# Kernel tuning notes

Hardware: AMD Instinct MI355X
Metric: run time of the kernel (lower is better)

The kernel has to match this reference:

```python
import jax, jax.numpy as jnp
import numpy as np

IN_CH = 128
OUT_CH = 256
KSIZE = 3
DOWN = 2
WSCALE_GAIN = 1.0
LR_MUL = 1.0
ACT_GAIN = float(np.sqrt(2.0))  # lrelu def_gain
CONV_CLAMP = 256.0
LRELU_SLOPE = 0.2


def _setup_filter():
    # upfirdn2d.setup_filter([1,3,3,1]): normalize 1D then outer product -> 2D
    f1 = jnp.asarray([1.0, 3.0, 3.0, 1.0], dtype=jnp.float32)
    f1 = f1 / jnp.sum(f1)
    f2 = jnp.outer(f1, f1)  # [4,4]
    return f2


def setup_inputs() -> dict:
    key = jax.random.key(0)
    k1, k2 = jax.random.split(key)
    x = jax.random.normal(k1, (16, IN_CH, 256, 256), dtype=jnp.float32)
    weight = jax.random.normal(k2, (OUT_CH, IN_CH, KSIZE, KSIZE), dtype=jnp.float32)
    bias = jnp.zeros((OUT_CH,), dtype=jnp.float32)
    return {"x": x, "weight": weight, "bias": bias}


def reference(x, weight, bias):
    # runtime_gain = 1.0
    fan_in = KSIZE * KSIZE * IN_CH
    wscale = WSCALE_GAIN / np.sqrt(fan_in) * LR_MUL  # use_wscale=True
    w = weight * jnp.float32(wscale)
    b = bias * jnp.float32(LR_MUL)

    # filter_padding for k=3, fh=fw=4, down=2 -> (2,2,2,2) as (left,right,top,bottom)
    pad = (KSIZE // 2 + (4 - DOWN + 1) // 2, KSIZE // 2 + (4 - DOWN) // 2)
    # upfirdn2d(x, f, down=1, padding): pad then correlate with flipped filter
    f2 = _setup_filter()
    f2 = f2[::-1, ::-1]  # flip (symmetric here, kept for faithfulness)
    C = x.shape[1]
    fk = jnp.broadcast_to(f2[None, None], (C, 1, 4, 4))  # depthwise kernel
    x = lax.pad_fn(x, pad) if False else jnp.pad(x, ((0, 0), (0, 0), (pad[1], pad[0]) if False else (pad[0], pad[1]), (pad[0], pad[1])))
    x = jax.lax.conv_general_dilated(
        x, fk, window_strides=(1, 1), padding='VALID',
        dimension_numbers=('NCHW', 'OIHW', 'NCHW'),
        feature_group_count=C)

    # strided conv2d, padding=0, stride=down
    x = jax.lax.conv_general_dilated(
        x, w, window_strides=(DOWN, DOWN), padding='VALID',
        dimension_numbers=('NCHW', 'OIHW', 'NCHW'))

    # fused bias + lrelu + gain + clamp
    x = x + b[None, :, None, None]
    x = jnp.where(x >= 0, x, x * jnp.float32(LRELU_SLOPE)) * jnp.float32(ACT_GAIN)
    x = jnp.clip(x, -jnp.float32(CONV_CLAMP), jnp.float32(CONV_CLAMP))
    return x
```

## Files before the change

### kernel.cpp

```cpp
#include <hip/hip_runtime.h>

typedef __attribute__((ext_vector_type(8))) short bf16x8;
typedef __attribute__((ext_vector_type(4))) float f32x4;
typedef __attribute__((ext_vector_type(2))) float f32x2;
typedef __attribute__((ext_vector_type(4))) unsigned int u32x4;

static __device__ __forceinline__ unsigned short f2bf(float f) {
    union { float f; unsigned u; } v; v.f = f;
    return (unsigned short)((v.u + 0x7FFFu + ((v.u >> 16) & 1u)) >> 16);
}

__global__ void prep_weights(const float* __restrict__ w, unsigned short* __restrict__ wp) {
    int t = blockIdx.x * 256 + threadIdx.x;
    const float wscale = 0.02946278254943948f;
    int cw = t & 31;
    int oc = (t >> 5) & 255;
    int cr = t >> 13;
    int ch = cr / 9;
    int rs = cr - ch * 9;
    int r  = rs / 3;
    int s  = rs - r * 3;
    int c  = ch * 32 + cw;
    wp[t] = f2bf(w[((oc * 128 + c) * 3 + r) * 3 + s] * wscale);
}

__global__ __launch_bounds__(256, 2)
void blur_pre(const float* __restrict__ x, unsigned* __restrict__ bm, unsigned* __restrict__ bs) {
    const int b = blockIdx.x;
    const int tband = b & 15;
    const int chpg  = (b >> 4) & 3;
    const int cg    = (b >> 6) & 3;
    const int n     = b >> 8;
    const int wv = threadIdx.x >> 6;
    const int L  = threadIdx.x & 63;
    const int chp = chpg * 4 + wv;
    const float* p0 = x + (size_t)(n * 128 + cg * 32 + 2 * chp) * 65536;
    const float* p1 = p0 + 65536;
    const int t0 = tband * 16;
    const int J0 = 4 * L;
    const bool L0 = (L == 0), L63 = (L == 63);
    const int colA = L0 ? 0 : (J0 - 2);
    const int colB = L63 ? 252 : (J0 + 2);
    unsigned* ob = bm + (size_t)((n * 4 + cg) * 16 + chp) * 65792;
    unsigned* os = bs + (size_t)((n * 4 + cg) * 16 + chp) * 257;

    float h0[4][4], h1[4][4], e0[4], e1[4];
    #pragma unroll
    for (int i = 0; i < 20; ++i) {
        const int xr  = t0 - 2 + i;
        const int xrc = xr < 0 ? 0 : (xr > 255 ? 255 : xr);
        const float rm = (xr == xrc) ? 0.125f : 0.f;
        const float* r0 = p0 + (xrc << 8);
        const float* r1 = p1 + (xrc << 8);
        f32x4 rA0, rB0, rA1, rB1;
        __builtin_memcpy(&rA0, r0 + colA, 16);
        __builtin_memcpy(&rB0, r0 + colB, 16);
        __builtin_memcpy(&rA1, r1 + colA, 16);
        __builtin_memcpy(&rB1, r1 + colB, 16);
        const float A0x = L0 ? 0.f : rA0.x, A0y = L0 ? 0.f : rA0.y;
        const float A0z = L0 ? rA0.x : rA0.z, A0w = L0 ? rA0.y : rA0.w;
        const float A1x = L0 ? 0.f : rA1.x, A1y = L0 ? 0.f : rA1.y;
        const float A1z = L0 ? rA1.x : rA1.z, A1w = L0 ? rA1.y : rA1.w;
        const float B0x = L63 ? rB0.z : rB0.x, B0y = L63 ? rB0.w : rB0.y;
        const float B0z = L63 ? 0.f : rB0.z,  B0w = L63 ? 0.f : rB0.w;
        const float B1x = L63 ? rB1.z : rB1.x, B1y = L63 ? rB1.w : rB1.y;
        const float B1z = L63 ? 0.f : rB1.z,  B1w = L63 ? 0.f : rB1.w;
        h0[0][i & 3] = (A0x + 3.f * (A0y + A0z) + A0w) * rm;
        h0[1][i & 3] = (A0y + 3.f * (A0z + A0w) + B0x) * rm;
        h0[2][i & 3] = (A0z + 3.f * (A0w + B0x) + B0y) * rm;
        h0[3][i & 3] = (A0w + 3.f * (B0x + B0y) + B0z) * rm;
        e0[i & 3]    = (B0x + 3.f * B0y) * rm;
        h1[0][i & 3] = (A1x + 3.f * (A1y + A1z) + A1w) * rm;
        h1[1][i & 3] = (A1y + 3.f * (A1z + A1w) + B1x) * rm;
        h1[2][i & 3] = (A1z + 3.f * (A1w + B1x) + B1y) * rm;
        h1[3][i & 3] = (A1w + 3.f * (B1x + B1y) + B1z) * rm;
        e1[i & 3]    = (B1x + 3.f * B1y) * rm;
        if (i >= 3) {
            const int t = t0 + i - 3;
            u32x4 o;
            #pragma unroll
            for (int d = 0; d < 4; ++d) {
                float bv0 = (h0[d][(i-3)&3] + 3.f*(h0[d][(i-2)&3] + h0[d][(i-1)&3]) + h0[d][i&3]) * 0.125f;
                float bv1 = (h1[d][(i-3)&3] + 3.f*(h1[d][(i-2)&3] + h1[d][(i-1)&3]) + h1[d][i&3]) * 0.125f;
                o[d] = (unsigned)f2bf(bv0) | ((unsigned)f2bf(bv1) << 16);
            }
            *(u32x4*)(ob + (size_t)t * 256 + J0) = o;
            if (L63) {
                float c0 = (e0[(i-3)&3] + 3.f*(e0[(i-2)&3] + e0[(i-1)&3]) + e0[i&3]) * 0.125f;
                float c1 = (e1[(i-3)&3] + 3.f*(e1[(i-2)&3] + e1[(i-1)&3]) + e1[i&3]) * 0.125f;
                os[t] = (unsigned)f2bf(c0) | ((unsigned)f2bf(c1) << 16);
            }
        }
    }
}

#define MF __builtin_amdgcn_mfma_f32_16x16x32_bf16
#define WLOAD(S0, S1, S2, S3, KOFF) {                                          \
    const unsigned short* _wn = wbase + (size_t)(KOFF) * 8192;                 \
    S0 = *(const bf16x8*)(_wn);        S1 = *(const bf16x8*)(_wn + 512);       \
    S2 = *(const bf16x8*)(_wn + 1024); S3 = *(const bf16x8*)(_wn + 1536);      \
}
#define CSTEP(ADRS, R, S0, S1, S2, S3) {                                       \
    const unsigned char* _ab = lds + (ADRS) + (R) * 2112;                      \
    bf16x8 a0 = *(const bf16x8*)(_ab);                                         \
    bf16x8 a1 = *(const bf16x8*)(_ab + 4224);                                  \
    bf16x8 a2 = *(const bf16x8*)(_ab + 8448);                                  \
    bf16x8 a3 = *(const bf16x8*)(_ab + 12672);                                 \
    __builtin_amdgcn_s_setprio(1);                                             \
    acc[0][0]=MF(a0,S0,acc[0][0],0,0,0); acc[0][1]=MF(a0,S1,acc[0][1],0,0,0);  \
    acc[0][2]=MF(a0,S2,acc[0][2],0,0,0); acc[0][3]=MF(a0,S3,acc[0][3],0,0,0);  \
    acc[1][0]=MF(a1,S0,acc[1][0],0,0,0); acc[1][1]=MF(a1,S1,acc[1][1],0,0,0);  \
    acc[1][2]=MF(a1,S2,acc[1][2],0,0,0); acc[1][3]=MF(a1,S3,acc[1][3],0,0,0);  \
    acc[2][0]=MF(a2,S0,acc[2][0],0,0,0); acc[2][1]=MF(a2,S1,acc[2][1],0,0,0);  \
    acc[2][2]=MF(a2,S2,acc[2][2],0,0,0); acc[2][3]=MF(a2,S3,acc[2][3],0,0,0);  \
    acc[3][0]=MF(a3,S0,acc[3][0],0,0,0); acc[3][1]=MF(a3,S1,acc[3][1],0,0,0);  \
    acc[3][2]=MF(a3,S2,acc[3][2],0,0,0); acc[3][3]=MF(a3,S3,acc[3][3],0,0,0);  \
    __builtin_amdgcn_s_setprio(0);                                             \
}
#define CHUNK(BASE, A0,A1,A2,A3, B0,B1,B2,B3)                                  \
    CSTEP(adr0, 0, A0,A1,A2,A3) WLOAD(A0,A1,A2,A3, (BASE)+2)                   \
    CSTEP(adr1, 0, B0,B1,B2,B3) WLOAD(B0,B1,B2,B3, (BASE)+3)                   \
    CSTEP(adr2, 0, A0,A1,A2,A3) WLOAD(A0,A1,A2,A3, (BASE)+4)                   \
    CSTEP(adr0, 1, B0,B1,B2,B3) WLOAD(B0,B1,B2,B3, (BASE)+5)                   \
    CSTEP(adr1, 1, A0,A1,A2,A3) WLOAD(A0,A1,A2,A3, (BASE)+6)                   \
    CSTEP(adr2, 1, B0,B1,B2,B3) WLOAD(B0,B1,B2,B3, (BASE)+7)                   \
    CSTEP(adr0, 2, A0,A1,A2,A3) WLOAD(A0,A1,A2,A3, (BASE)+8)                   \
    CSTEP(adr1, 2, B0,B1,B2,B3) WLOAD(B0,B1,B2,B3, (BASE)+9)                   \
    CSTEP(adr2, 2, A0,A1,A2,A3) WLOAD(A0,A1,A2,A3, (BASE)+10)
#define CHUNK_LAST(BASE, A0,A1,A2,A3, B0,B1,B2,B3)                             \
    CSTEP(adr0, 0, A0,A1,A2,A3) WLOAD(A0,A1,A2,A3, (BASE)+2)                   \
    CSTEP(adr1, 0, B0,B1,B2,B3) WLOAD(B0,B1,B2,B3, (BASE)+3)                   \
    CSTEP(adr2, 0, A0,A1,A2,A3) WLOAD(A0,A1,A2,A3, (BASE)+4)                   \
    CSTEP(adr0, 1, B0,B1,B2,B3) WLOAD(B0,B1,B2,B3, (BASE)+5)                   \
    CSTEP(adr1, 1, A0,A1,A2,A3) WLOAD(A0,A1,A2,A3, (BASE)+6)                   \
    CSTEP(adr2, 1, B0,B1,B2,B3) WLOAD(B0,B1,B2,B3, (BASE)+7)                   \
    CSTEP(adr0, 2, A0,A1,A2,A3) WLOAD(A0,A1,A2,A3, (BASE)+8)                   \
    CSTEP(adr1, 2, B0,B1,B2,B3)                                                \
    CSTEP(adr2, 2, A0,A1,A2,A3)

__global__ __launch_bounds__(512, 2)
void conv_stage2(const unsigned* __restrict__ bm, const unsigned* __restrict__ bs,
                 const unsigned short* __restrict__ wp, const float* __restrict__ bias,
                 float* __restrict__ out) {
    __shared__ __align__(16) unsigned char lds[35904];

    const int bx = blockIdx.x;
    const int n  = bx >> 7;
    const int tt = bx & 127;
    const int u0 = (tt >> 3) * 8;
    const int v0 = (tt & 7) * 16;

    const int tid  = threadIdx.x;
    const int lane = tid & 63;
    const int wid  = tid >> 6;
    const int wm   = wid >> 2;
    const int wn   = wid & 3;
    const int g    = lane >> 4;
    const int wq   = lane & 15;

    unsigned goffm[5], ldsa[5];
    bool act[5], isq8[5], sside[5];
    #pragma unroll
    for (int ii = 0; ii < 5; ++ii) {
        int k = tid + 512 * ii;
        act[ii] = (k < 2448);
        int kk = act[ii] ? k : 0;
        int pr = kk / 9;
        int Jq = kk - 9 * pr;
        int chp = pr & 15;
        int row = pr >> 4;
        int t = 2 * u0 + row;
        isq8[ii]  = (Jq == 8);
        sside[ii] = isq8[ii] && (v0 == 112);
        if (Jq < 8) {
            goffm[ii] = (unsigned)((chp * 257 + t) << 8) + (unsigned)(2 * v0 + 4 * Jq);
            ldsa[ii]  = (unsigned)(row * 2112 + Jq * 256
                       + (((chp >> 2) ^ (Jq & 3)) << 4) + (chp & 3) * 4);
        } else {
            goffm[ii] = sside[ii] ? (unsigned)(chp * 257 + t)
                                  : (unsigned)((chp * 257 + t) << 8) + (unsigned)(2 * v0 + 32);
            ldsa[ii]  = (unsigned)(row * 2112 + 2048 + ((chp >> 2) << 4) + (chp & 3) * 4);
        }
    }
    const unsigned* bmn = bm + (size_t)(n * 4) * 16 * 65792;
    const unsigned* bsn = bs + (size_t)(n * 4) * 16 * 257;
    u32x4 SV[5];

#define STAGE_LOAD(CG) {                                                       \
    const unsigned* _m = bmn + (size_t)(CG) * 16 * 65792;                      \
    const unsigned* _s = bsn + (size_t)(CG) * 16 * 257;                        \
    _Pragma("unroll")                                                          \
    for (int ii = 0; ii < 5; ++ii) {                                           \
        if (act[ii]) {                                                         \
            if (!isq8[ii]) { __builtin_memcpy(&SV[ii], _m + goffm[ii], 16); }  \
            else { SV[ii].x = sside[ii] ? _s[goffm[ii]] : _m[goffm[ii]]; }     \
        }                                                                      \
    }                                                                          \
}
#define STAGE_WRITE() {                                                        \
    _Pragma("unroll")                                                          \
    for (int ii = 0; ii < 5; ++ii) {                                           \
        if (act[ii]) {                                                         \
            if (!isq8[ii]) {                                                   \
                *(unsigned*)(lds + ldsa[ii])       = SV[ii].x;                 \
                *(unsigned*)(lds + ldsa[ii] + 64)  = SV[ii].y;                 \
                *(unsigned*)(lds + ldsa[ii] + 192) = SV[ii].z;                 \
                *(unsigned*)(lds + ldsa[ii] + 128) = SV[ii].w;                 \
            } else {                                                           \
                *(unsigned*)(lds + ldsa[ii]) = SV[ii].x;                       \
            }                                                                  \
        }                                                                      \
    }                                                                          \
}

    unsigned adr0, adr1, adr2;
    {
        #pragma unroll
        for (int s = 0; s < 3; ++s) {
            unsigned bj = 2u * (unsigned)wq + (unsigned)s;
            unsigned av = (bj ^ ((bj >> 1) & 1u)) * 64u
                        + (((unsigned)g ^ ((bj >> 2) & 3u)) << 4) + (unsigned)wm * 16896u;
            if (s == 0) adr0 = av; else if (s == 1) adr1 = av; else adr2 = av;
        }
    }

    const unsigned short* wbase = wp + (size_t)(wn * 64 + wq) * 32 + g * 8;
    bf16x8 WA0, WA1, WA2, WA3, WB0, WB1, WB2, WB3;
    WLOAD(WA0, WA1, WA2, WA3, 0)
    WLOAD(WB0, WB1, WB2, WB3, 1)

    f32x4 acc[4][4];
    #pragma unroll
    for (int i = 0; i < 4; ++i)
        #pragma unroll
        for (int j = 0; j < 4; ++j)
            acc[i][j] = (f32x4){0.f, 0.f, 0.f, 0.f};

    STAGE_LOAD(0)
    STAGE_WRITE()
    __syncthreads();
    STAGE_LOAD(1)
    CHUNK(0, WA0, WA1, WA2, WA3, WB0, WB1, WB2, WB3)
    __syncthreads();
    STAGE_WRITE()
    __syncthreads();
    STAGE_LOAD(2)
    CHUNK(9, WB0, WB1, WB2, WB3, WA0, WA1, WA2, WA3)
    __syncthreads();
    STAGE_WRITE()
    __syncthreads();
    STAGE_LOAD(3)
    CHUNK(18, WA0, WA1, WA2, WA3, WB0, WB1, WB2, WB3)
    __syncthreads();
    STAGE_WRITE()
    __syncthreads();
    CHUNK_LAST(27, WB0, WB1, WB2, WB3, WA0, WA1, WA2, WA3)

    const float gain = 1.4142135623730951f;
    #pragma unroll
    for (int nf = 0; nf < 4; ++nf) {
        const int ocg = wn * 64 + nf * 16 + wq;
        const float bb = bias[ocg];
        #pragma unroll
        for (int mf = 0; mf < 4; ++mf) {
            int u = u0 + wm * 4 + mf;
            f32x4 o;
            #pragma unroll
            for (int i = 0; i < 4; ++i) {
                float z = acc[mf][nf][i] + bb;
                z = (z >= 0.f ? z : 0.2f * z) * gain;
                o[i] = fminf(fmaxf(z, -256.f), 256.f);
            }
            *(f32x4*)(out + (((size_t)n * 256 + ocg) * 128 + u) * 128 + v0 + 4 * g) = o;
        }
    }
}

#define FROW(row) {                                                            \
    int xr  = xr0 + (row);                                                     \
    int xrc = xr < 0 ? 0 : (xr > 255 ? 255 : xr);                              \
    float rm = (xr == xrc) ? 0.125f : 0.0f;                                    \
    const float* p = q + (xrc << 8);                                           \
    f32x4 lo; f32x2 hi;                                                        \
    __builtin_memcpy(&lo, p, 16);                                              \
    __builtin_memcpy(&hi, p + 4, 8);                                           \
    hA[(row) & 3] = (lo.x + 3.f * (lo.y + lo.z) + lo.w) * rm;                  \
    hB[(row) & 3] = (lo.y + 3.f * (lo.z + lo.w) + hi.x) * rm;                  \
    hC[(row) & 3] = (lo.z + 3.f * (lo.w + hi.x) + hi.y) * rm;                  \
}
#define SROW(row) {                                                            \
    int xr = xr0 + (row);                                                      \
    float wv0=0.f,wv1=0.f,wv2=0.f,wv3=0.f,wv4=0.f,wv5=0.f;                     \
    if ((unsigned)xr < 256u) {                                                 \
        const float* p = q + (xr << 8);                                        \
        if ((unsigned)(wc + 0) < 256u) wv0 = p[0];                             \
        if ((unsigned)(wc + 1) < 256u) wv1 = p[1];                             \
        if ((unsigned)(wc + 2) < 256u) wv2 = p[2];                             \
        if ((unsigned)(wc + 3) < 256u) wv3 = p[3];                             \
        if ((unsigned)(wc + 4) < 256u) wv4 = p[4];                             \
        if ((unsigned)(wc + 5) < 256u) wv5 = p[5];                             \
    }                                                                          \
    hA[(row) & 3] = (wv0 + 3.f * (wv1 + wv2) + wv3) * 0.125f;                  \
    hB[(row) & 3] = (wv1 + 3.f * (wv2 + wv3) + wv4) * 0.125f;                  \
    hC[(row) & 3] = (wv2 + 3.f * (wv3 + wv4) + wv5) * 0.125f;                  \
}
#define VROW(row) {                                                            \
    float bv0 = (hA[(row - 3) & 3] + 3.f * (hA[(row - 2) & 3] + hA[(row - 1) & 3]) + hA[(row) & 3]) * 0.125f; \
    float bv1 = (hB[(row - 3) & 3] + 3.f * (hB[(row - 2) & 3] + hB[(row - 1) & 3]) + hB[(row) & 3]) * 0.125f; \
    unsigned rb = (unsigned)(row - 3) * 2640u;                                 \
    *(unsigned short*)(flds + rb + o0) = f2bf(bv0);                            \
    *(unsigned short*)(flds + rb + o1) = f2bf(bv1);                            \
    if (a == 15) {                                                             \
        float bv2 = (hC[(row - 3) & 3] + 3.f * (hC[(row - 2) & 3] + hC[(row - 1) & 3]) + hC[(row) & 3]) * 0.125f; \
        *(unsigned short*)(flds + rb + o2) = f2bf(bv2);                        \
    }                                                                          \
}
__global__ __launch_bounds__(512, 4)
void conv_blur_mfma(const float* __restrict__ x, const unsigned short* __restrict__ wp,
                    const float* __restrict__ bias, float* __restrict__ out) {
    __shared__ __align__(16) unsigned char flds[17 * 33 * 80];
    const int bx = blockIdx.x;
    const int n  = bx >> 7;
    const int tt = bx & 127;
    const int u0 = (tt >> 3) * 8;
    const int v0 = (tt & 7) * 16;
    const int tid  = threadIdx.x;
    const int lane = tid & 63;
    const int wid  = tid >> 6;
    const int wm   = wid >> 2;
    const int wn   = wid & 3;
    const int g    = lane >> 4;
    const int wq   = lane & 15;
    const int a   = tid & 15;
    const int chl = tid >> 4;
    const int wc  = 2 * v0 - 2 + 2 * a;
    const bool edge = (v0 == 0 && a == 0) || (v0 == 112 && a == 15);
    const float* planeBase = x + (size_t)(n * 128 + chl) * 65536;
    const int xr0 = 2 * u0 - 2;
    const unsigned chpart = (unsigned)(((chl >> 1) & 3) * 4 + (chl & 1) * 2);
    const unsigned q4 = (unsigned)(chl >> 3);
    const int c0 = 2 * a;
    const unsigned o0 = (unsigned)(c0 + 0) * 80u + ((q4 ^ (((unsigned)(c0 + 0) >> 3) & 3u)) << 4) + chpart;
    const unsigned o1 = (unsigned)(c0 + 1) * 80u + ((q4 ^ (((unsigned)(c0 + 1) >> 3) & 3u)) << 4) + chpart;
    const unsigned o2 = (unsigned)(c0 + 2) * 80u + ((q4 ^ (((unsigned)(c0 + 2) >> 3) & 3u)) << 4) + chpart;
    const unsigned short* wpL = wp + (size_t)(wn * 64 + wq) * 32 + g * 8;
    f32x4 acc[4][4];
    #pragma unroll
    for (int i = 0; i < 4; ++i)
        #pragma unroll
        for (int j = 0; j < 4; ++j)
            acc[i][j] = (f32x4){0.f, 0.f, 0.f, 0.f};
    for (int ch = 0; ch < 4; ++ch) {
        const float* q = planeBase + (size_t)ch * 32 * 65536 + wc;
        float hA[4], hB[4], hC[4];
        if (!edge) { FROW(0) FROW(1) FROW(2) }
        else       { SROW(0) SROW(1) SROW(2) }
        __syncthreads();
        if (!edge) {
            #pragma unroll
            for (int row = 3; row < 20; ++row) { FROW(row) VROW(row) }
        } else {
            #pragma unroll
            for (int row = 3; row < 20; ++row) { SROW(row) VROW(row) }
        }
        __syncthreads();
        const unsigned short* wpc = wpL + (size_t)ch * 9 * 8192;
        #pragma unroll 1
        for (int r = 0; r < 3; ++r) {
            #pragma unroll 1
            for (int s = 0; s < 3; ++s) {
                bf16x8 b0 = *(const bf16x8*)(wpc + 0 * 512);
                bf16x8 b1 = *(const bf16x8*)(wpc + 1 * 512);
                bf16x8 b2 = *(const bf16x8*)(wpc + 2 * 512);
                bf16x8 b3 = *(const bf16x8*)(wpc + 3 * 512);
                wpc += 8192;
                int bj = 2 * wq + s;
                unsigned cb = (unsigned)bj * 80u + ((unsigned)(g ^ ((bj >> 3) & 3)) << 4);
                #pragma unroll
                for (int mf = 0; mf < 4; ++mf) {
                    int bi = 2 * (wm * 4 + mf) + r;
                    bf16x8 afrag = *(const bf16x8*)(flds + (unsigned)bi * 2640u + cb);
                    acc[mf][0] = MF(afrag, b0, acc[mf][0], 0, 0, 0);
                    acc[mf][1] = MF(afrag, b1, acc[mf][1], 0, 0, 0);
                    acc[mf][2] = MF(afrag, b2, acc[mf][2], 0, 0, 0);
                    acc[mf][3] = MF(afrag, b3, acc[mf][3], 0, 0, 0);
                }
            }
        }
    }
    const float gain = 1.4142135623730951f;
    #pragma unroll
    for (int nf = 0; nf < 4; ++nf) {
        int ocg = wn * 64 + nf * 16 + wq;
        float bv = bias[ocg];
        #pragma unroll
        for (int mf = 0; mf < 4; ++mf) {
            int u = u0 + wm * 4 + mf;
            f32x4 o;
            #pragma unroll
            for (int i = 0; i < 4; ++i) {
                float z = acc[mf][nf][i] + bv;
                z = (z >= 0.f ? z : 0.2f * z) * gain;
                o[i] = fminf(fmaxf(z, -256.f), 256.f);
            }
            *(f32x4*)(out + (((size_t)n * 256 + ocg) * 128 + u) * 128 + v0 + 4 * g) = o;
        }
    }
}

extern "C" void kernel_launch(void* const* d_in, const int* in_sizes, int n_in,
                              void* d_out, int out_size, void* d_ws, size_t ws_size,
                              hipStream_t stream) {
    const float* x    = (const float*)d_in[0];
    const float* w    = (const float*)d_in[1];
    const float* bias = (const float*)d_in[2];
    unsigned short* wp = (unsigned short*)d_ws;
    float* out = (float*)d_out;

    const size_t BM_BYTES = 269484032u;
    const size_t BS_BYTES = 1052672u;
    const size_t NEED = 589824u + BM_BYTES + BS_BYTES;
    prep_weights<<<1152, 256, 0, stream>>>(w, wp);
    if (ws_size >= NEED) {
        unsigned* bm = (unsigned*)((unsigned char*)d_ws + 589824);
        unsigned* bs = (unsigned*)((unsigned char*)d_ws + 589824 + BM_BYTES);
        blur_pre<<<4096, 256, 0, stream>>>(x, bm, bs);
        conv_stage2<<<2048, 512, 0, stream>>>(bm, bs, wp, bias, out);
    } else {
        conv_blur_mfma<<<2048, 512, 0, stream>>>(x, wp, bias, out);
    }
}
```

Measured before the change: 461.2 us.

## Double-buffer LDS in conv stage, merge blur side column, remap blur blocks

The conv stage now uses two LDS buffers, so the next channel group's staged data is written while the current buffer is consumed, dropping one barrier per stage. The blurred intermediate row stride grows from 256 to 260 words so the extra right-edge column sits inline, removing the separate side buffer and its branch in the loader. blur_pre remaps block indices to interleave work across channel groups and skips a row computation that is never stored. Doubling LDS to about 70KB per block may limit occupancy at two blocks per CU.

```diff
diff --git a/kernel.cpp b/kernel.cpp
--- a/kernel.cpp
+++ b/kernel.cpp
@@ -25,8 +25,9 @@
 }
 
 __global__ __launch_bounds__(256, 2)
-void blur_pre(const float* __restrict__ x, unsigned* __restrict__ bm, unsigned* __restrict__ bs) {
-    const int b = blockIdx.x;
+void blur_pre(const float* __restrict__ x, unsigned* __restrict__ bm) {
+    const int braw = blockIdx.x;
+    const int b = ((braw & 7) << 9) | (braw >> 3);
     const int tband = b & 15;
     const int chpg  = (b >> 4) & 3;
     const int cg    = (b >> 6) & 3;
@@ -41,12 +42,12 @@
     const bool L0 = (L == 0), L63 = (L == 63);
     const int colA = L0 ? 0 : (J0 - 2);
     const int colB = L63 ? 252 : (J0 + 2);
-    unsigned* ob = bm + (size_t)((n * 4 + cg) * 16 + chp) * 65792;
-    unsigned* os = bs + (size_t)((n * 4 + cg) * 16 + chp) * 257;
+    unsigned* ob = bm + (size_t)((n * 4 + cg) * 16 + chp) * 66820u;
 
     float h0[4][4], h1[4][4], e0[4], e1[4];
     #pragma unroll
     for (int i = 0; i < 20; ++i) {
+        if (i == 19 && tband != 15) break;
         const int xr  = t0 - 2 + i;
         const int xrc = xr < 0 ? 0 : (xr > 255 ? 255 : xr);
         const float rm = (xr == xrc) ? 0.125f : 0.f;
@@ -62,9 +63,9 @@
         const float A1x = L0 ? 0.f : rA1.x, A1y = L0 ? 0.f : rA1.y;
         const float A1z = L0 ? rA1.x : rA1.z, A1w = L0 ? rA1.y : rA1.w;
         const float B0x = L63 ? rB0.z : rB0.x, B0y = L63 ? rB0.w : rB0.y;
-        const float B0z = L63 ? 0.f : rB0.z,  B0w = L63 ? 0.f : rB0.w;
+        const float B0z = L63 ? 0.f : rB0.z;
         const float B1x = L63 ? rB1.z : rB1.x, B1y = L63 ? rB1.w : rB1.y;
-        const float B1z = L63 ? 0.f : rB1.z,  B1w = L63 ? 0.f : rB1.w;
+        const float B1z = L63 ? 0.f : rB1.z;
         h0[0][i & 3] = (A0x + 3.f * (A0y + A0z) + A0w) * rm;
         h0[1][i & 3] = (A0y + 3.f * (A0z + A0w) + B0x) * rm;
         h0[2][i & 3] = (A0z + 3.f * (A0w + B0x) + B0y) * rm;
@@ -84,11 +85,11 @@
                 float bv1 = (h1[d][(i-3)&3] + 3.f*(h1[d][(i-2)&3] + h1[d][(i-1)&3]) + h1[d][i&3]) * 0.125f;
                 o[d] = (unsigned)f2bf(bv0) | ((unsigned)f2bf(bv1) << 16);
             }
-            *(u32x4*)(ob + (size_t)t * 256 + J0) = o;
+            *(u32x4*)(ob + (size_t)t * 260 + J0) = o;
             if (L63) {
                 float c0 = (e0[(i-3)&3] + 3.f*(e0[(i-2)&3] + e0[(i-1)&3]) + e0[i&3]) * 0.125f;
                 float c1 = (e1[(i-3)&3] + 3.f*(e1[(i-2)&3] + e1[(i-1)&3]) + e1[i&3]) * 0.125f;
-                os[t] = (unsigned)f2bf(c0) | ((unsigned)f2bf(c1) << 16);
+                ob[(size_t)t * 260 + 256] = (unsigned)f2bf(c0) | ((unsigned)f2bf(c1) << 16);
             }
         }
     }
@@ -100,8 +101,8 @@
     S0 = *(const bf16x8*)(_wn);        S1 = *(const bf16x8*)(_wn + 512);       \
     S2 = *(const bf16x8*)(_wn + 1024); S3 = *(const bf16x8*)(_wn + 1536);      \
 }
-#define CSTEP(ADRS, R, S0, S1, S2, S3) {                                       \
-    const unsigned char* _ab = lds + (ADRS) + (R) * 2112;                      \
+#define CSTEP(BUF, ADRS, R, S0, S1, S2, S3) {                                  \
+    const unsigned char* _ab = lds + (BUF) + (ADRS) + (R) * 2112;              \
     bf16x8 a0 = *(const bf16x8*)(_ab);                                         \
     bf16x8 a1 = *(const bf16x8*)(_ab + 4224);                                  \
     bf16x8 a2 = *(const bf16x8*)(_ab + 8448);                                  \
@@ -117,32 +118,31 @@
     acc[3][2]=MF(a3,S2,acc[3][2],0,0,0); acc[3][3]=MF(a3,S3,acc[3][3],0,0,0);  \
     __builtin_amdgcn_s_setprio(0);                                             \
 }
-#define CHUNK(BASE, A0,A1,A2,A3, B0,B1,B2,B3)                                  \
-    CSTEP(adr0, 0, A0,A1,A2,A3) WLOAD(A0,A1,A2,A3, (BASE)+2)                   \
-    CSTEP(adr1, 0, B0,B1,B2,B3) WLOAD(B0,B1,B2,B3, (BASE)+3)                   \
-    CSTEP(adr2, 0, A0,A1,A2,A3) WLOAD(A0,A1,A2,A3, (BASE)+4)                   \
-    CSTEP(adr0, 1, B0,B1,B2,B3) WLOAD(B0,B1,B2,B3, (BASE)+5)                   \
-    CSTEP(adr1, 1, A0,A1,A2,A3) WLOAD(A0,A1,A2,A3, (BASE)+6)                   \
-    CSTEP(adr2, 1, B0,B1,B2,B3) WLOAD(B0,B1,B2,B3, (BASE)+7)                   \
-    CSTEP(adr0, 2, A0,A1,A2,A3) WLOAD(A0,A1,A2,A3, (BASE)+8)                   \
-    CSTEP(adr1, 2, B0,B1,B2,B3) WLOAD(B0,B1,B2,B3, (BASE)+9)                   \
-    CSTEP(adr2, 2, A0,A1,A2,A3) WLOAD(A0,A1,A2,A3, (BASE)+10)
-#define CHUNK_LAST(BASE, A0,A1,A2,A3, B0,B1,B2,B3)                             \
-    CSTEP(adr0, 0, A0,A1,A2,A3) WLOAD(A0,A1,A2,A3, (BASE)+2)                   \
-    CSTEP(adr1, 0, B0,B1,B2,B3) WLOAD(B0,B1,B2,B3, (BASE)+3)                   \
-    CSTEP(adr2, 0, A0,A1,A2,A3) WLOAD(A0,A1,A2,A3, (BASE)+4)                   \
-    CSTEP(adr0, 1, B0,B1,B2,B3) WLOAD(B0,B1,B2,B3, (BASE)+5)                   \
-    CSTEP(adr1, 1, A0,A1,A2,A3) WLOAD(A0,A1,A2,A3, (BASE)+6)                   \
-    CSTEP(adr2, 1, B0,B1,B2,B3) WLOAD(B0,B1,B2,B3, (BASE)+7)                   \
-    CSTEP(adr0, 2, A0,A1,A2,A3) WLOAD(A0,A1,A2,A3, (BASE)+8)                   \
-    CSTEP(adr1, 2, B0,B1,B2,B3)                                                \
-    CSTEP(adr2, 2, A0,A1,A2,A3)
+#define CHUNK(BUF, BASE, A0,A1,A2,A3, B0,B1,B2,B3)                             \
+    CSTEP(BUF, adr0, 0, A0,A1,A2,A3) WLOAD(A0,A1,A2,A3, (BASE)+2)              \
+    CSTEP(BUF, adr1, 0, B0,B1,B2,B3) WLOAD(B0,B1,B2,B3, (BASE)+3)              \
+    CSTEP(BUF, adr2, 0, A0,A1,A2,A3) WLOAD(A0,A1,A2,A3, (BASE)+4)              \
+    CSTEP(BUF, adr0, 1, B0,B1,B2,B3) WLOAD(B0,B1,B2,B3, (BASE)+5)              \
+    CSTEP(BUF, adr1, 1, A0,A1,A2,A3) WLOAD(A0,A1,A2,A3, (BASE)+6)              \
+    CSTEP(BUF, adr2, 1, B0,B1,B2,B3) WLOAD(B0,B1,B2,B3, (BASE)+7)              \
+    CSTEP(BUF, adr0, 2, A0,A1,A2,A3) WLOAD(A0,A1,A2,A3, (BASE)+8)              \
+    CSTEP(BUF, adr1, 2, B0,B1,B2,B3) WLOAD(B0,B1,B2,B3, (BASE)+9)              \
+    CSTEP(BUF, adr2, 2, A0,A1,A2,A3) WLOAD(A0,A1,A2,A3, (BASE)+10)
+#define CHUNK_LAST(BUF, BASE, A0,A1,A2,A3, B0,B1,B2,B3)                        \
+    CSTEP(BUF, adr0, 0, A0,A1,A2,A3) WLOAD(A0,A1,A2,A3, (BASE)+2)              \
+    CSTEP(BUF, adr1, 0, B0,B1,B2,B3) WLOAD(B0,B1,B2,B3, (BASE)+3)              \
+    CSTEP(BUF, adr2, 0, A0,A1,A2,A3) WLOAD(A0,A1,A2,A3, (BASE)+4)              \
+    CSTEP(BUF, adr0, 1, B0,B1,B2,B3) WLOAD(B0,B1,B2,B3, (BASE)+5)              \
+    CSTEP(BUF, adr1, 1, A0,A1,A2,A3) WLOAD(A0,A1,A2,A3, (BASE)+6)              \
+    CSTEP(BUF, adr2, 1, B0,B1,B2,B3) WLOAD(B0,B1,B2,B3, (BASE)+7)              \
+    CSTEP(BUF, adr0, 2, A0,A1,A2,A3) WLOAD(A0,A1,A2,A3, (BASE)+8)              \
+    CSTEP(BUF, adr1, 2, B0,B1,B2,B3)                                           \
+    CSTEP(BUF, adr2, 2, A0,A1,A2,A3)
 
 __global__ __launch_bounds__(512, 2)
-void conv_stage2(const unsigned* __restrict__ bm, const unsigned* __restrict__ bs,
-                 const unsigned short* __restrict__ wp, const float* __restrict__ bias,
-                 float* __restrict__ out) {
-    __shared__ __align__(16) unsigned char lds[35904];
+void conv_stage2(const unsigned* __restrict__ bm, const unsigned short* __restrict__ wp,
+                 const float* __restrict__ bias, float* __restrict__ out) {
+    __shared__ __align__(16) unsigned char lds[2 * 35904];
 
     const int bx = blockIdx.x;
     const int n  = bx >> 7;
@@ -159,7 +159,7 @@
     const int wq   = lane & 15;
 
     unsigned goffm[5], ldsa[5];
-    bool act[5], isq8[5], sside[5];
+    bool act[5], isq8[5];
     #pragma unroll
     for (int ii = 0; ii < 5; ++ii) {
         int k = tid + 512 * ii;
@@ -170,44 +170,40 @@
         int chp = pr & 15;
         int row = pr >> 4;
         int t = 2 * u0 + row;
-        isq8[ii]  = (Jq == 8);
-        sside[ii] = isq8[ii] && (v0 == 112);
+        isq8[ii] = (Jq == 8);
+        int col = isq8[ii] ? (2 * v0 + 32) : (2 * v0 + 4 * Jq);
+        goffm[ii] = (unsigned)((chp * 257 + t) * 260 + col);
         if (Jq < 8) {
-            goffm[ii] = (unsigned)((chp * 257 + t) << 8) + (unsigned)(2 * v0 + 4 * Jq);
-            ldsa[ii]  = (unsigned)(row * 2112 + Jq * 256
-                       + (((chp >> 2) ^ (Jq & 3)) << 4) + (chp & 3) * 4);
+            ldsa[ii] = (unsigned)(row * 2112 + Jq * 256
+                     + (((chp >> 2) ^ (Jq & 3)) << 4) + (chp & 3) * 4);
         } else {
-            goffm[ii] = sside[ii] ? (unsigned)(chp * 257 + t)
-                                  : (unsigned)((chp * 257 + t) << 8) + (unsigned)(2 * v0 + 32);
-            ldsa[ii]  = (unsigned)(row * 2112 + 2048 + ((chp >> 2) << 4) + (chp & 3) * 4);
-        }
-    }
-    const unsigned* bmn = bm + (size_t)(n * 4) * 16 * 65792;
-    const unsigned* bsn = bs + (size_t)(n * 4) * 16 * 257;
+            ldsa[ii] = (unsigned)(row * 2112 + 2048 + ((chp >> 2) << 4) + (chp & 3) * 4);
+        }
+    }
+    const unsigned* bmn = bm + (size_t)(n * 4) * 16 * 66820u;
     u32x4 SV[5];
 
 #define STAGE_LOAD(CG) {                                                       \
-    const unsigned* _m = bmn + (size_t)(CG) * 16 * 65792;                      \
-    const unsigned* _s = bsn + (size_t)(CG) * 16 * 257;                        \
+    const unsigned* _m = bmn + (size_t)(CG) * 16 * 66820u;                     \
     _Pragma("unroll")                                                          \
     for (int ii = 0; ii < 5; ++ii) {                                           \
         if (act[ii]) {                                                         \
-            if (!isq8[ii]) { __builtin_memcpy(&SV[ii], _m + goffm[ii], 16); }  \
-            else { SV[ii].x = sside[ii] ? _s[goffm[ii]] : _m[goffm[ii]]; }     \
+            if (!isq8[ii]) { SV[ii] = *(const u32x4*)(_m + goffm[ii]); }       \
+            else { SV[ii].x = _m[goffm[ii]]; }                                 \
         }                                                                      \
     }                                                                          \
 }
-#define STAGE_WRITE() {                                                        \
+#define STAGE_WRITE(BUF) {                                                     \
     _Pragma("unroll")                                                          \
     for (int ii = 0; ii < 5; ++ii) {                                           \
         if (act[ii]) {                                                         \
             if (!isq8[ii]) {                                                   \
-                *(unsigned*)(lds + ldsa[ii])       = SV[ii].x;                 \
-                *(unsigned*)(lds + ldsa[ii] + 64)  = SV[ii].y;                 \
-                *(unsigned*)(lds + ldsa[ii] + 192) = SV[ii].z;                 \
-                *(unsigned*)(lds + ldsa[ii] + 128) = SV[ii].w;                 \
+                *(unsigned*)(lds + (BUF) + ldsa[ii])       = SV[ii].x;         \
+                *(unsigned*)(lds + (BUF) + ldsa[ii] + 64)  = SV[ii].y;         \
+                *(unsigned*)(lds + (BUF) + ldsa[ii] + 192) = SV[ii].z;         \
+                *(unsigned*)(lds + (BUF) + ldsa[ii] + 128) = SV[ii].w;         \
             } else {                                                           \
-                *(unsigned*)(lds + ldsa[ii]) = SV[ii].x;                       \
+                *(unsigned*)(lds + (BUF) + ldsa[ii]) = SV[ii].x;               \
             }                                                                  \
         }                                                                      \
     }                                                                          \
@@ -237,24 +233,25 @@
             acc[i][j] = (f32x4){0.f, 0.f, 0.f, 0.f};
 
     STAGE_LOAD(0)
-    STAGE_WRITE()
+    STAGE_WRITE(0)
     __syncthreads();
     STAGE_LOAD(1)
-    CHUNK(0, WA0, WA1, WA2, WA3, WB0, WB1, WB2, WB3)
-    __syncthreads();
-    STAGE_WRITE()
+
+    CHUNK(0, 0, WA0, WA1, WA2, WA3, WB0, WB1, WB2, WB3)
+    STAGE_WRITE(35904)
     __syncthreads();
     STAGE_LOAD(2)
-    CHUNK(9, WB0, WB1, WB2, WB3, WA0, WA1, WA2, WA3)
-    __syncthreads();
-    STAGE_WRITE()
+
+    CHUNK(35904, 9, WB0, WB1, WB2, WB3, WA0, WA1, WA2, WA3)
+    STAGE_WRITE(0)
     __syncthreads();
     STAGE_LOAD(3)
-    CHUNK(18, WA0, WA1, WA2, WA3, WB0, WB1, WB2, WB3)
+
+    CHUNK(0, 18, WA0, WA1, WA2, WA3, WB0, WB1, WB2, WB3)
+    STAGE_WRITE(35904)
     __syncthreads();
-    STAGE_WRITE()
-    __syncthreads();
-    CHUNK_LAST(27, WB0, WB1, WB2, WB3, WA0, WA1, WA2, WA3)
+
+    CHUNK_LAST(35904, 27, WB0, WB1, WB2, WB3, WA0, WA1, WA2, WA3)
 
     const float gain = 1.4142135623730951f;
     #pragma unroll
@@ -417,15 +414,13 @@
     unsigned short* wp = (unsigned short*)d_ws;
     float* out = (float*)d_out;
 
-    const size_t BM_BYTES = 269484032u;
-    const size_t BS_BYTES = 1052672u;
-    const size_t NEED = 589824u + BM_BYTES + BS_BYTES;
+    const size_t BM_BYTES = (size_t)1024 * 66820 * 4;
+    const size_t NEED = 589824u + BM_BYTES;
     prep_weights<<<1152, 256, 0, stream>>>(w, wp);
     if (ws_size >= NEED) {
         unsigned* bm = (unsigned*)((unsigned char*)d_ws + 589824);
-        unsigned* bs = (unsigned*)((unsigned char*)d_ws + 589824 + BM_BYTES);
-        blur_pre<<<4096, 256, 0, stream>>>(x, bm, bs);
-        conv_stage2<<<2048, 512, 0, stream>>>(bm, bs, wp, bias, out);
+        blur_pre<<<4096, 256, 0, stream>>>(x, bm);
+        conv_stage2<<<2048, 512, 0, stream>>>(bm, wp, bias, out);
     } else {
         conv_blur_mfma<<<2048, 512, 0, stream>>>(x, wp, bias, out);
     }
```

Result: no change. 466.1 us (+1.1%).
